# Performance work log

Measured on AMD Instinct MI355X. Metric: run time of the kernel, lower is better.

The kernel has to match this reference:

```python
import jax, jax.numpy as jnp
import numpy as np
import math

B, L, D, H, DFF = 2, 2048, 1024, 16, 4096

def _mha(xq, xkv, Wq, bq, Wk, bk, Wv, bv, Wo, bo, mask, h):
    # xq: [B,Lq,D], xkv: [B,Lk,D], mask: [B,1,Lq,Lk] bool
    b, lq, d = xq.shape
    dk = d // h
    q = (xq @ Wq + bq).reshape(b, lq, h, dk).transpose(0, 2, 1, 3)        # [B,h,Lq,dk]
    k = (xkv @ Wk + bk).reshape(b, -1, h, dk).transpose(0, 2, 1, 3)       # [B,h,Lk,dk]
    v = (xkv @ Wv + bv).reshape(b, -1, h, dk).transpose(0, 2, 1, 3)       # [B,h,Lk,dk]
    scores = jnp.einsum('bhqd,bhkd->bhqk', q, k) / jnp.sqrt(jnp.float32(dk))
    scores = jnp.where(mask, scores, jnp.float32(-1e9))                   # masked_fill(mask==0, -1e9)
    prob = jax.nn.softmax(scores, axis=-1)
    out = jnp.einsum('bhqk,bhkd->bhqd', prob, v)
    out = out.transpose(0, 2, 1, 3).reshape(b, lq, d)
    return out @ Wo + bo

def setup_inputs() -> dict:
    key = jax.random.key(0)
    ks = jax.random.split(key, 16)
    s = 0.02
    inp = {
        'tgt': jax.random.normal(ks[0], (B, L, D), jnp.float32),
        'encoder_out': jax.random.normal(ks[1], (B, L, D), jnp.float32),
        'tgt_mask': jnp.broadcast_to(jnp.tril(jnp.ones((L, L), bool)), (B, 1, L, L)),
        'src_tgt_mask': jnp.ones((B, 1, L, L), bool),
    }
    names = ['sWq','sWk','sWv','sWo','cWq','cWk','cWv','cWo']
    for i, n in enumerate(names):
        inp[n] = s * jax.random.normal(ks[2 + i], (D, D), jnp.float32)
        inp['sb' + n[2] if n[0] == 's' else 'cb' + n[2]] = jnp.zeros((D,), jnp.float32)
    inp['W1'] = s * jax.random.normal(ks[10], (D, DFF), jnp.float32)
    inp['b1'] = jnp.zeros((DFF,), jnp.float32)
    inp['W2'] = s * jax.random.normal(ks[11], (DFF, D), jnp.float32)
    inp['b2'] = jnp.zeros((D,), jnp.float32)
    return inp

def reference(tgt, encoder_out, tgt_mask, src_tgt_mask,
              sWq, sbq, sWk, sbk, sWv, sbv, sWo, sbo,
              cWq, cbq, cWk, cbk, cWv, cbv, cWo, cbo,
              W1, b1, W2, b2):
    # residual 1: masked self-attention (no norm)
    x = tgt + _mha(tgt, tgt, sWq, sbq, sWk, sbk, sWv, sbv, sWo, sbo, tgt_mask, H)
    # residual 2: cross-attention over encoder_out
    x = x + _mha(x, encoder_out, cWq, cbq, cWk, cbk, cWv, cbv, cWo, cbo, src_tgt_mask, H)
    # residual 3: position-wise FFN with ReLU
    x = x + (jax.nn.relu(x @ W1 + b1) @ W2 + b2)
    return x
```

## Files before the change

### kernel.cpp

```cpp
#include <hip/hip_runtime.h>

typedef unsigned short u16;
typedef __attribute__((ext_vector_type(8))) short short8;
typedef __attribute__((ext_vector_type(8))) __bf16 bf16x8;
typedef __attribute__((ext_vector_type(4))) float f32x4;
typedef __attribute__((ext_vector_type(4))) u16 u16x4;

#define GLD16(gp, lp) __builtin_amdgcn_global_load_lds( \
    (const __attribute__((address_space(1))) unsigned int*)(gp), \
    (__attribute__((address_space(3))) unsigned int*)(lp), 16, 0, 0)

__device__ __forceinline__ float bf2f(u16 u){
  unsigned x = ((unsigned)u) << 16; float f; __builtin_memcpy(&f, &x, 4); return f;
}
__device__ __forceinline__ u16 f2bf(float f){
  unsigned x; __builtin_memcpy(&x, &f, 4);
  x += 0x7fffu + ((x >> 16) & 1u);
  return (u16)(x >> 16);
}
__device__ __forceinline__ f32x4 mfma_bf16(short8 a, short8 b, f32x4 c){
  return __builtin_amdgcn_mfma_f32_16x16x32_bf16(
      __builtin_bit_cast(bf16x8, a), __builtin_bit_cast(bf16x8, b), c, 0, 0, 0);
}

__global__ __launch_bounds__(256) void k_conv(const float* __restrict__ s, u16* __restrict__ d, int n){
  int i4 = (blockIdx.x * 256 + threadIdx.x) * 4;
  if (i4 < n){
    float4 v = *(const float4*)(s + i4);
    u16x4 o; o.x = f2bf(v.x); o.y = f2bf(v.y); o.z = f2bf(v.z); o.w = f2bf(v.w);
    *(u16x4*)(d + i4) = o;
  }
}

__global__ __launch_bounds__(256) void k_transpose(const float* __restrict__ s, u16* __restrict__ d, int K, int N){
  __shared__ float t[32][33];
  int bx = blockIdx.x * 32, by = blockIdx.y * 32;
  int x = threadIdx.x & 31, y = threadIdx.x >> 5;
  #pragma unroll
  for (int i = 0; i < 4; i++)
    t[y + i*8][x] = s[(size_t)(by + y + i*8) * N + bx + x];
  __syncthreads();
  #pragma unroll
  for (int i = 0; i < 4; i++)
    d[(size_t)(bx + y + i*8) * K + by + x] = f2bf(t[x][y + i*8]);
}

struct TP8 { const float* s[8]; u16* d[8]; };
__global__ __launch_bounds__(256) void k_transpose8(TP8 p){
  __shared__ float t[32][33];
  const float* s = p.s[blockIdx.z];
  u16* d = p.d[blockIdx.z];
  int bx = blockIdx.x * 32, by = blockIdx.y * 32;
  int x = threadIdx.x & 31, y = threadIdx.x >> 5;
  #pragma unroll
  for (int i = 0; i < 4; i++)
    t[y + i*8][x] = s[(size_t)(by + y + i*8) * 1024 + bx + x];
  __syncthreads();
  #pragma unroll
  for (int i = 0; i < 4; i++)
    d[(size_t)(bx + y + i*8) * 1024 + by + x] = f2bf(t[x][y + i*8]);
}

__global__ __launch_bounds__(256) void k_packbias(
    const float* __restrict__ sbq, const float* __restrict__ sbk,
    const float* __restrict__ sbv, const float* __restrict__ cbk,
    const float* __restrict__ cbv, float* __restrict__ pbS,
    float* __restrict__ pbC){
  int i = blockIdx.x * 256 + threadIdx.x;
  if (i < 3072) pbS[i] = (i < 1024) ? sbq[i] : (i < 2048 ? sbk[i-1024] : sbv[i-2048]);
  if (i < 2048) pbC[i] = (i < 1024) ? cbk[i] : cbv[i-1024];
}

template<int EPI>
__global__ __launch_bounds__(256, 2) void k_gemm_bt(
    const u16* __restrict__ A, const u16* __restrict__ BT,
    const float* __restrict__ bias,
    u16* __restrict__ outB, int M, int N, int K,
    int vt_start, u16* __restrict__ Vt){
  __shared__ u16 As[128*32];
  __shared__ u16 Bs[128*32];
  int tid = threadIdx.x, wave = tid >> 6, lane = tid & 63;
  int bm = blockIdx.x * 128, bn = blockIdx.y * 128;
  int wm = (wave & 1) * 64, wn = (wave >> 1) * 64;
  int l15 = lane & 15, quad = lane >> 4;

  f32x4 z = {0.f, 0.f, 0.f, 0.f};
  f32x4 acc[4][4];
  #pragma unroll
  for (int a = 0; a < 4; a++)
    #pragma unroll
    for (int b = 0; b < 4; b++) acc[a][b] = z;

  int sr = wave*16 + (lane >> 2);
  int sc = (lane & 3) * 8;
  const u16* Ag = A  + (size_t)(bm + sr) * K + sc;
  const u16* Bg = BT + (size_t)(bn + sr) * K + sc;

  for (int k0 = 0; k0 < K; k0 += 32){
    #pragma unroll
    for (int i = 0; i < 2; i++){
      GLD16(Ag + (size_t)i*64*K + k0, &As[(wave*16 + i*64) * 32]);
      GLD16(Bg + (size_t)i*64*K + k0, &Bs[(wave*16 + i*64) * 32]);
    }
    __syncthreads();
    short8 af[4], bf[4];
    #pragma unroll
    for (int mi = 0; mi < 4; mi++)
      af[mi] = *(const short8*)&As[(wm + mi*16 + l15)*32 + quad*8];
    #pragma unroll
    for (int ni = 0; ni < 4; ni++)
      bf[ni] = *(const short8*)&Bs[(wn + ni*16 + l15)*32 + quad*8];
    #pragma unroll
    for (int mi = 0; mi < 4; mi++)
      #pragma unroll
      for (int ni = 0; ni < 4; ni++)
        acc[mi][ni] = mfma_bf16(af[mi], bf[ni], acc[mi][ni]);
    __syncthreads();
  }

  #pragma unroll
  for (int mi = 0; mi < 4; mi++){
    #pragma unroll
    for (int ni = 0; ni < 4; ni++){
      int col = bn + wn + ni*16 + l15;
      float bv = bias[col];
      if (col >= vt_start){
        int vc = col - vt_start;
        int hh = vc >> 6, dd = vc & 63;
        int row0 = bm + wm + mi*16 + quad*4;
        int bb = row0 >> 11, ll = row0 & 2047;
        u16x4 vv;
        #pragma unroll
        for (int r = 0; r < 4; r++) vv[r] = f2bf(acc[mi][ni][r] + bv);
        *(u16x4*)&Vt[(((size_t)bb*16 + hh)*64 + dd)*2048 + ll] = vv;
      } else {
        #pragma unroll
        for (int r = 0; r < 4; r++){
          int row = bm + wm + mi*16 + quad*4 + r;
          float v = acc[mi][ni][r] + bv;
          if (EPI == 1) v = v > 0.f ? v : 0.f;
          outB[(size_t)row * N + col] = f2bf(v);
        }
      }
    }
  }
}

template<int EPI>
__global__ __launch_bounds__(256, 4) void k_gemm_bt64(
    const u16* __restrict__ A, const u16* __restrict__ BT,
    const float* __restrict__ bias, const float* __restrict__ resid,
    float* __restrict__ outF, u16* __restrict__ outB,
    int M, int N, int K){
  __shared__ u16 As[128*32];
  __shared__ u16 Bs[64*32];
  int tid = threadIdx.x, wave = tid >> 6, lane = tid & 63;
  int bm = blockIdx.x * 128, bn = blockIdx.y * 64;
  int wm = wave * 32;
  int l15 = lane & 15, quad = lane >> 4;

  f32x4 z = {0.f, 0.f, 0.f, 0.f};
  f32x4 acc[2][4];
  #pragma unroll
  for (int a = 0; a < 2; a++)
    #pragma unroll
    for (int b = 0; b < 4; b++) acc[a][b] = z;

  int sr = wave*16 + (lane >> 2);
  int sc = (lane & 3) * 8;
  const u16* Ag = A  + (size_t)(bm + sr) * K + sc;
  const u16* Bg = BT + (size_t)(bn + sr) * K + sc;

  for (int k0 = 0; k0 < K; k0 += 32){
    #pragma unroll
    for (int i = 0; i < 2; i++)
      GLD16(Ag + (size_t)i*64*K + k0, &As[(wave*16 + i*64) * 32]);
    GLD16(Bg + k0, &Bs[(wave*16) * 32]);
    __syncthreads();
    short8 af[2], bf[4];
    #pragma unroll
    for (int mi = 0; mi < 2; mi++)
      af[mi] = *(const short8*)&As[(wm + mi*16 + l15)*32 + quad*8];
    #pragma unroll
    for (int ni = 0; ni < 4; ni++)
      bf[ni] = *(const short8*)&Bs[(ni*16 + l15)*32 + quad*8];
    #pragma unroll
    for (int mi = 0; mi < 2; mi++)
      #pragma unroll
      for (int ni = 0; ni < 4; ni++)
        acc[mi][ni] = mfma_bf16(af[mi], bf[ni], acc[mi][ni]);
    __syncthreads();
  }

  #pragma unroll
  for (int mi = 0; mi < 2; mi++){
    #pragma unroll
    for (int ni = 0; ni < 4; ni++){
      int col = bn + ni*16 + l15;
      float bv = bias[col];
      #pragma unroll
      for (int r = 0; r < 4; r++){
        int row = bm + wm + mi*16 + quad*4 + r;
        float v = acc[mi][ni][r] + bv;
        size_t idx = (size_t)row * N + col;
        if (EPI >= 2) v += resid[idx];
        if (EPI == 2 || EPI == 3) outF[idx] = v;
        if (EPI != 3) outB[idx] = f2bf(v);
      }
    }
  }
}

template<bool CAUSAL>
__global__ __launch_bounds__(256, 2) void k_flash(
    const u16* __restrict__ Q, int ldq,
    const u16* __restrict__ Kg, int ldk,
    const u16* __restrict__ Vt,
    u16* __restrict__ O, int ldo){
  __shared__ u16 Ks[128*64];
  __shared__ u16 Vs[64*128];
  __shared__ u16 Ps[128*128];
  int tid = threadIdx.x, wave = tid >> 6, lane = tid & 63;
  int l15 = lane & 15, quad = lane >> 4;
  int qt = blockIdx.x;
  int bh = blockIdx.y;
  int b = bh >> 4, h = bh & 15;
  size_t bL = (size_t)b * 2048;
  const u16* qp = Q  + (bL + qt*128) * (size_t)ldq + h*64;
  const u16* kp = Kg + bL * (size_t)ldk + h*64;
  const u16* vtp = Vt + (size_t)bh * 64 * 2048;
  int wm = wave * 32;

  short8 qf[2][2];
  #pragma unroll
  for (int mi = 0; mi < 2; mi++)
    #pragma unroll
    for (int ks = 0; ks < 2; ks++){
      short8 t = *(const short8*)(qp + (size_t)(wm + mi*16 + l15)*ldq + ks*32 + quad*8);
      #pragma unroll
      for (int j = 0; j < 8; j++)
        t[j] = (short)f2bf(bf2f((u16)t[j]) * 0.125f);
      qf[mi][ks] = t;
    }

  f32x4 z = {0.f, 0.f, 0.f, 0.f};
  f32x4 o[2][4];
  float mrow[2], lrow[2];
  #pragma unroll
  for (int mi = 0; mi < 2; mi++){ mrow[mi] = -3.0e38f; lrow[mi] = 0.f; }
  #pragma unroll
  for (int mi = 0; mi < 2; mi++)
    #pragma unroll
    for (int nd = 0; nd < 4; nd++) o[mi][nd] = z;

  int nkt = CAUSAL ? (qt + 1) : 16;
  for (int kt = 0; kt < nkt; kt++){
    int cg = ((lane & 7) ^ ((lane >> 3) & 7)) * 8;
    #pragma unroll
    for (int i = 0; i < 4; i++){
      int r = i*32 + wave*8 + (lane >> 3);
      GLD16(kp + (size_t)(kt*128 + r) * ldk + cg, &Ks[(i*32 + wave*8) * 64]);
    }
    {
      int d = tid >> 2;
      int cbase = tid & 3;
      const u16* vrow = vtp + (size_t)d*2048 + kt*128;
      short8 vv[4];
      #pragma unroll
      for (int i = 0; i < 4; i++)
        vv[i] = *(const short8*)(vrow + (cbase + i*4)*8);
      #pragma unroll
      for (int i = 0; i < 4; i++){
        int c = cbase + i*4;
        int phys = (c & 8) | ((c ^ (d & 7)) & 7);
        *(short8*)&Vs[d*128 + phys*8] = vv[i];
      }
    }
    __syncthreads();

    f32x4 s[2][8];
    #pragma unroll
    for (int mi = 0; mi < 2; mi++)
      #pragma unroll
      for (int nk = 0; nk < 8; nk++) s[mi][nk] = z;
    #pragma unroll
    for (int ks = 0; ks < 2; ks++){
      short8 kf[8];
      #pragma unroll
      for (int nk = 0; nk < 8; nk++){
        int row = nk*16 + l15;
        kf[nk] = *(const short8*)&Ks[row*64 + (((ks*4 + quad) ^ (row & 7)))*8];
      }
      #pragma unroll
      for (int mi = 0; mi < 2; mi++)
        #pragma unroll
        for (int nk = 0; nk < 8; nk++)
          s[mi][nk] = mfma_bf16(kf[nk], qf[mi][ks], s[mi][nk]);
    }

    if (CAUSAL && kt == qt){
      #pragma unroll
      for (int mi = 0; mi < 2; mi++){
        int q = wm + mi*16 + l15;
        #pragma unroll
        for (int nk = 0; nk < 8; nk++)
          #pragma unroll
          for (int r = 0; r < 4; r++){
            int key = nk*16 + quad*4 + r;
            if (key > q) s[mi][nk][r] = -1e30f;
          }
      }
    }

    #pragma unroll
    for (int mi = 0; mi < 2; mi++){
      float mx = s[mi][0][0];
      #pragma unroll
      for (int nk = 0; nk < 8; nk++)
        #pragma unroll
        for (int r = 0; r < 4; r++) mx = fmaxf(mx, s[mi][nk][r]);
      mx = fmaxf(mx, __shfl_xor(mx, 16));
      mx = fmaxf(mx, __shfl_xor(mx, 32));
      float mnew = fmaxf(mrow[mi], mx);
      float alpha = __expf(mrow[mi] - mnew);
      mrow[mi] = mnew;
      float ls = 0.f;
      #pragma unroll
      for (int nk = 0; nk < 8; nk++)
        #pragma unroll
        for (int r = 0; r < 4; r++){
          float p = __expf(s[mi][nk][r] - mnew);
          s[mi][nk][r] = p;
          ls += p;
        }
      ls += __shfl_xor(ls, 16);
      ls += __shfl_xor(ls, 32);
      lrow[mi] = lrow[mi] * alpha + ls;
      #pragma unroll
      for (int r = 0; r < 4; r++){
        float ar = __shfl(alpha, quad*20 + r);
        #pragma unroll
        for (int nd = 0; nd < 4; nd++) o[mi][nd][r] *= ar;
      }
    }

    #pragma unroll
    for (int mi = 0; mi < 2; mi++){
      int row = wm + mi*16 + l15;
      #pragma unroll
      for (int nk = 0; nk < 8; nk++){
        u16x4 pw;
        #pragma unroll
        for (int r = 0; r < 4; r++) pw[r] = f2bf(s[mi][nk][r]);
        int c = nk*4 + quad;
        int phys = c ^ (row & 14);
        *(u16x4*)&Ps[row*128 + phys*4] = pw;
      }
    }

    #pragma unroll
    for (int kc = 0; kc < 4; kc++){
      short8 vf[4], pf[2];
      #pragma unroll
      for (int nd = 0; nd < 4; nd++){
        int d = nd*16 + l15;
        int cc = kc*4 + quad;
        int phys = (cc & 8) | ((cc ^ (d & 7)) & 7);
        vf[nd] = *(const short8*)&Vs[d*128 + phys*8];
      }
      #pragma unroll
      for (int mi = 0; mi < 2; mi++){
        int row = wm + mi*16 + l15;
        int c = kc*8 + quad*2;
        int phys = c ^ (row & 14);
        pf[mi] = *(const short8*)&Ps[row*128 + phys*4];
      }
      #pragma unroll
      for (int mi = 0; mi < 2; mi++)
        #pragma unroll
        for (int nd = 0; nd < 4; nd++)
          o[mi][nd] = mfma_bf16(pf[mi], vf[nd], o[mi][nd]);
    }
    __syncthreads();
  }

  u16* op = O + (bL + qt*128) * (size_t)ldo + h*64;
  #pragma unroll
  for (int mi = 0; mi < 2; mi++){
    float invl = 1.f / lrow[mi];
    #pragma unroll
    for (int r = 0; r < 4; r++){
      float ir = __shfl(invl, quad*20 + r);
      #pragma unroll
      for (int nd = 0; nd < 4; nd++)
        op[(size_t)(wm + mi*16 + quad*4 + r)*ldo + nd*16 + l15] = f2bf(o[mi][nd][r] * ir);
    }
  }
}

extern "C" void kernel_launch(void* const* d_in, const int* in_sizes, int n_in,
                              void* d_out, int out_size, void* d_ws, size_t ws_size,
                              hipStream_t stream){
  (void)in_sizes; (void)n_in; (void)out_size; (void)ws_size;
  const float* tgt = (const float*)d_in[0];
  const float* enc = (const float*)d_in[1];
  const float* sWq = (const float*)d_in[4];  const float* sbq = (const float*)d_in[5];
  const float* sWk = (const float*)d_in[6];  const float* sbk = (const float*)d_in[7];
  const float* sWv = (const float*)d_in[8];  const float* sbv = (const float*)d_in[9];
  const float* sWo = (const float*)d_in[10]; const float* sbo = (const float*)d_in[11];
  const float* cWq = (const float*)d_in[12]; const float* cbq = (const float*)d_in[13];
  const float* cWk = (const float*)d_in[14]; const float* cbk = (const float*)d_in[15];
  const float* cWv = (const float*)d_in[16]; const float* cbv = (const float*)d_in[17];
  const float* cWo = (const float*)d_in[18]; const float* cbo = (const float*)d_in[19];
  const float* W1  = (const float*)d_in[20]; const float* b1  = (const float*)d_in[21];
  const float* W2  = (const float*)d_in[22]; const float* b2  = (const float*)d_in[23];
  float* out = (float*)d_out;

  const int M = 4096;
  const int NEVER = 1 << 30;
  char* w = (char*)d_ws;
  auto alloc = [&](size_t bytes)->void*{ void* p = w; w += (bytes + 255) & ~(size_t)255; return p; };
  u16* tb    = (u16*)alloc((size_t)M*1024*2);
  u16* eb    = (u16*)alloc((size_t)M*1024*2);
  u16* qkv   = (u16*)alloc((size_t)M*3072*2);
  u16* ao    = (u16*)alloc((size_t)M*1024*2);
  u16* xb    = (u16*)alloc((size_t)M*1024*2);
  float* x1f = (float*)alloc((size_t)M*1024*4);
  u16* hbuf  = (u16*)alloc((size_t)M*4096*2);
  u16* VtS   = (u16*)alloc((size_t)32*64*2048*2);
  u16* VtC   = (u16*)alloc((size_t)32*64*2048*2);
  u16* sQKVT = (u16*)alloc((size_t)3072*1024*2);
  u16* sWoT  = (u16*)alloc((size_t)1024*1024*2);
  u16* cWqT  = (u16*)alloc((size_t)1024*1024*2);
  u16* cKVT  = (u16*)alloc((size_t)2048*1024*2);
  u16* cWoT  = (u16*)alloc((size_t)1024*1024*2);
  u16* W1T   = (u16*)alloc((size_t)4096*1024*2);
  u16* W2T   = (u16*)alloc((size_t)1024*4096*2);
  float* pbS = (float*)alloc(3072*4);
  float* pbC = (float*)alloc(2048*4);
  u16* cq  = tb;
  u16* ckv = qkv;

  k_conv<<<dim3(4096), 256, 0, stream>>>(tgt, tb, M*1024);
  k_conv<<<dim3(4096), 256, 0, stream>>>(enc, eb, M*1024);
  TP8 tp;
  tp.s[0]=sWq; tp.s[1]=sWk; tp.s[2]=sWv; tp.s[3]=sWo;
  tp.s[4]=cWq; tp.s[5]=cWk; tp.s[6]=cWv; tp.s[7]=cWo;
  tp.d[0]=sQKVT; tp.d[1]=sQKVT+1024*1024; tp.d[2]=sQKVT+2048*1024; tp.d[3]=sWoT;
  tp.d[4]=cWqT; tp.d[5]=cKVT; tp.d[6]=cKVT+1024*1024; tp.d[7]=cWoT;
  k_transpose8<<<dim3(32,32,8), 256, 0, stream>>>(tp);
  k_transpose<<<dim3(128,32), 256, 0, stream>>>(W1, W1T, 1024, 4096);
  k_transpose<<<dim3(32,128), 256, 0, stream>>>(W2, W2T, 4096, 1024);
  k_packbias<<<dim3(12), 256, 0, stream>>>(sbq, sbk, sbv, cbk, cbv, pbS, pbC);

  k_gemm_bt<0><<<dim3(32,24), 256, 0, stream>>>(tb, sQKVT, pbS, qkv, M, 3072, 1024, 2048, VtS);
  k_flash<true><<<dim3(16,32), 256, 0, stream>>>(qkv, 3072, qkv+1024, 3072, VtS, ao, 1024);
  k_gemm_bt64<2><<<dim3(32,16), 256, 0, stream>>>(ao, sWoT, sbo, tgt, x1f, xb, M, 1024, 1024);

  k_gemm_bt64<0><<<dim3(32,16), 256, 0, stream>>>(xb, cWqT, cbq, nullptr, nullptr, cq, M, 1024, 1024);
  k_gemm_bt<0><<<dim3(32,16), 256, 0, stream>>>(eb, cKVT, pbC, ckv, M, 2048, 1024, 1024, VtC);
  k_flash<false><<<dim3(16,32), 256, 0, stream>>>(cq, 1024, ckv, 2048, VtC, ao, 1024);
  k_gemm_bt64<2><<<dim3(32,16), 256, 0, stream>>>(ao, cWoT, cbo, x1f, x1f, xb, M, 1024, 1024);

  k_gemm_bt<1><<<dim3(32,32), 256, 0, stream>>>(xb, W1T, b1, hbuf, M, 4096, 1024, NEVER, nullptr);
  k_gemm_bt64<3><<<dim3(32,16), 256, 0, stream>>>(hbuf, W2T, b2, x1f, out, nullptr, M, 1024, 4096);
}
```

Baseline: 589.8 us.

## Double-buffer GEMM, unify N=1024 GEMMs, and tune flash softmax and loads

Makes the 128x128 GEMM double-buffered in LDS, issuing the next K-tile's global-to-LDS loads before computing on the current one so only one barrier per iteration remains. The 128x64 GEMM is removed and the N=1024 projections run on the 128x128 kernel with residual epilogues. In flash attention, log2(e) is folded into the Q scale so softmax uses raw exp2, P is packed to bf16 by truncation via perm instead of round-to-nearest, V tiles are loaded with direct global-to-LDS loads, and causal query tiles are interleaved to balance work. Larger tiles for the N=1024 GEMMs mean fewer blocks (256 versus 512) and more LDS per block, and truncating P slightly changes numerics.

```diff
diff --git a/kernel.cpp b/kernel.cpp
--- a/kernel.cpp
+++ b/kernel.cpp
@@ -1,14 +1,25 @@
 #include <hip/hip_runtime.h>
 
 typedef unsigned short u16;
+typedef unsigned int u32;
 typedef __attribute__((ext_vector_type(8))) short short8;
 typedef __attribute__((ext_vector_type(8))) __bf16 bf16x8;
 typedef __attribute__((ext_vector_type(4))) float f32x4;
 typedef __attribute__((ext_vector_type(4))) u16 u16x4;
+typedef __attribute__((ext_vector_type(2))) u32 u32x2;
 
 #define GLD16(gp, lp) __builtin_amdgcn_global_load_lds( \
     (const __attribute__((address_space(1))) unsigned int*)(gp), \
     (__attribute__((address_space(3))) unsigned int*)(lp), 16, 0, 0)
+
+#if defined(__has_builtin) && __has_builtin(__builtin_amdgcn_exp2f)
+#define EXP2(x) __builtin_amdgcn_exp2f(x)
+#else
+static __device__ __forceinline__ float exp2_asm(float x){
+  float r; asm("v_exp_f32 %0, %1" : "=v"(r) : "v"(x)); return r;
+}
+#define EXP2(x) exp2_asm(x)
+#endif
 
 __device__ __forceinline__ float bf2f(u16 u){
   unsigned x = ((unsigned)u) << 16; float f; __builtin_memcpy(&f, &x, 4); return f;
@@ -17,6 +28,10 @@
   unsigned x; __builtin_memcpy(&x, &f, 4);
   x += 0x7fffu + ((x >> 16) & 1u);
   return (u16)(x >> 16);
+}
+__device__ __forceinline__ u32 pkhi(float lo, float hi){
+  u32 a, b; __builtin_memcpy(&a, &lo, 4); __builtin_memcpy(&b, &hi, 4);
+  return __builtin_amdgcn_perm(b, a, 0x07060302u);
 }
 __device__ __forceinline__ f32x4 mfma_bf16(short8 a, short8 b, f32x4 c){
   return __builtin_amdgcn_mfma_f32_16x16x32_bf16(
@@ -74,11 +89,11 @@
 template<int EPI>
 __global__ __launch_bounds__(256, 2) void k_gemm_bt(
     const u16* __restrict__ A, const u16* __restrict__ BT,
-    const float* __restrict__ bias,
-    u16* __restrict__ outB, int M, int N, int K,
-    int vt_start, u16* __restrict__ Vt){
-  __shared__ u16 As[128*32];
-  __shared__ u16 Bs[128*32];
+    const float* __restrict__ bias, const float* __restrict__ resid,
+    float* __restrict__ outF, u16* __restrict__ outB,
+    int M, int N, int K, int vt_start, u16* __restrict__ Vt){
+  __shared__ u16 As[2][128*32];
+  __shared__ u16 Bs[2][128*32];
   int tid = threadIdx.x, wave = tid >> 6, lane = tid & 63;
   int bm = blockIdx.x * 128, bn = blockIdx.y * 128;
   int wm = (wave & 1) * 64, wn = (wave >> 1) * 64;
@@ -95,27 +110,35 @@
   int sc = (lane & 3) * 8;
   const u16* Ag = A  + (size_t)(bm + sr) * K + sc;
   const u16* Bg = BT + (size_t)(bn + sr) * K + sc;
-
-  for (int k0 = 0; k0 < K; k0 += 32){
-    #pragma unroll
-    for (int i = 0; i < 2; i++){
-      GLD16(Ag + (size_t)i*64*K + k0, &As[(wave*16 + i*64) * 32]);
-      GLD16(Bg + (size_t)i*64*K + k0, &Bs[(wave*16 + i*64) * 32]);
-    }
+  int NK = K >> 5;
+
+  GLD16(Ag,                 &As[0][(wave*16     ) * 32]);
+  GLD16(Ag + (size_t)64*K,  &As[0][(wave*16 + 64) * 32]);
+  GLD16(Bg,                 &Bs[0][(wave*16     ) * 32]);
+  GLD16(Bg + (size_t)64*K,  &Bs[0][(wave*16 + 64) * 32]);
+
+  for (int kt = 0; kt < NK; kt++){
     __syncthreads();
+    int cur = kt & 1;
+    if (kt + 1 < NK){
+      int nb = cur ^ 1, k0 = (kt + 1) * 32;
+      GLD16(Ag + k0,                &As[nb][(wave*16     ) * 32]);
+      GLD16(Ag + (size_t)64*K + k0, &As[nb][(wave*16 + 64) * 32]);
+      GLD16(Bg + k0,                &Bs[nb][(wave*16     ) * 32]);
+      GLD16(Bg + (size_t)64*K + k0, &Bs[nb][(wave*16 + 64) * 32]);
+    }
     short8 af[4], bf[4];
     #pragma unroll
     for (int mi = 0; mi < 4; mi++)
-      af[mi] = *(const short8*)&As[(wm + mi*16 + l15)*32 + quad*8];
+      af[mi] = *(const short8*)&As[cur][(wm + mi*16 + l15)*32 + quad*8];
     #pragma unroll
     for (int ni = 0; ni < 4; ni++)
-      bf[ni] = *(const short8*)&Bs[(wn + ni*16 + l15)*32 + quad*8];
+      bf[ni] = *(const short8*)&Bs[cur][(wn + ni*16 + l15)*32 + quad*8];
     #pragma unroll
     for (int mi = 0; mi < 4; mi++)
       #pragma unroll
       for (int ni = 0; ni < 4; ni++)
         acc[mi][ni] = mfma_bf16(af[mi], bf[ni], acc[mi][ni]);
-    __syncthreads();
   }
 
   #pragma unroll
@@ -124,7 +147,7 @@
     for (int ni = 0; ni < 4; ni++){
       int col = bn + wn + ni*16 + l15;
       float bv = bias[col];
-      if (col >= vt_start){
+      if (EPI == 0 && col >= vt_start){
         int vc = col - vt_start;
         int hh = vc >> 6, dd = vc & 63;
         int row0 = bm + wm + mi*16 + quad*4;
@@ -139,73 +162,11 @@
           int row = bm + wm + mi*16 + quad*4 + r;
           float v = acc[mi][ni][r] + bv;
           if (EPI == 1) v = v > 0.f ? v : 0.f;
-          outB[(size_t)row * N + col] = f2bf(v);
+          size_t idx = (size_t)row * N + col;
+          if (EPI >= 2) v += resid[idx];
+          if (EPI == 2 || EPI == 3) outF[idx] = v;
+          if (EPI != 3) outB[idx] = f2bf(v);
         }
-      }
-    }
-  }
-}
-
-template<int EPI>
-__global__ __launch_bounds__(256, 4) void k_gemm_bt64(
-    const u16* __restrict__ A, const u16* __restrict__ BT,
-    const float* __restrict__ bias, const float* __restrict__ resid,
-    float* __restrict__ outF, u16* __restrict__ outB,
-    int M, int N, int K){
-  __shared__ u16 As[128*32];
-  __shared__ u16 Bs[64*32];
-  int tid = threadIdx.x, wave = tid >> 6, lane = tid & 63;
-  int bm = blockIdx.x * 128, bn = blockIdx.y * 64;
-  int wm = wave * 32;
-  int l15 = lane & 15, quad = lane >> 4;
-
-  f32x4 z = {0.f, 0.f, 0.f, 0.f};
-  f32x4 acc[2][4];
-  #pragma unroll
-  for (int a = 0; a < 2; a++)
-    #pragma unroll
-    for (int b = 0; b < 4; b++) acc[a][b] = z;
-
-  int sr = wave*16 + (lane >> 2);
-  int sc = (lane & 3) * 8;
-  const u16* Ag = A  + (size_t)(bm + sr) * K + sc;
-  const u16* Bg = BT + (size_t)(bn + sr) * K + sc;
-
-  for (int k0 = 0; k0 < K; k0 += 32){
-    #pragma unroll
-    for (int i = 0; i < 2; i++)
-      GLD16(Ag + (size_t)i*64*K + k0, &As[(wave*16 + i*64) * 32]);
-    GLD16(Bg + k0, &Bs[(wave*16) * 32]);
-    __syncthreads();
-    short8 af[2], bf[4];
-    #pragma unroll
-    for (int mi = 0; mi < 2; mi++)
-      af[mi] = *(const short8*)&As[(wm + mi*16 + l15)*32 + quad*8];
-    #pragma unroll
-    for (int ni = 0; ni < 4; ni++)
-      bf[ni] = *(const short8*)&Bs[(ni*16 + l15)*32 + quad*8];
-    #pragma unroll
-    for (int mi = 0; mi < 2; mi++)
-      #pragma unroll
-      for (int ni = 0; ni < 4; ni++)
-        acc[mi][ni] = mfma_bf16(af[mi], bf[ni], acc[mi][ni]);
-    __syncthreads();
-  }
-
-  #pragma unroll
-  for (int mi = 0; mi < 2; mi++){
-    #pragma unroll
-    for (int ni = 0; ni < 4; ni++){
-      int col = bn + ni*16 + l15;
-      float bv = bias[col];
-      #pragma unroll
-      for (int r = 0; r < 4; r++){
-        int row = bm + wm + mi*16 + quad*4 + r;
-        float v = acc[mi][ni][r] + bv;
-        size_t idx = (size_t)row * N + col;
-        if (EPI >= 2) v += resid[idx];
-        if (EPI == 2 || EPI == 3) outF[idx] = v;
-        if (EPI != 3) outB[idx] = f2bf(v);
       }
     }
   }
@@ -222,7 +183,8 @@
   __shared__ u16 Ps[128*128];
   int tid = threadIdx.x, wave = tid >> 6, lane = tid & 63;
   int l15 = lane & 15, quad = lane >> 4;
-  int qt = blockIdx.x;
+  int bx = blockIdx.x;
+  int qt = CAUSAL ? ((bx & 1) ? (15 - (bx >> 1)) : (bx >> 1)) : bx;
   int bh = blockIdx.y;
   int b = bh >> 4, h = bh & 15;
   size_t bL = (size_t)b * 2048;
@@ -231,6 +193,7 @@
   const u16* vtp = Vt + (size_t)bh * 64 * 2048;
   int wm = wave * 32;
 
+  const float QSCALE = 0.125f * 1.44269504088896f;
   short8 qf[2][2];
   #pragma unroll
   for (int mi = 0; mi < 2; mi++)
@@ -239,7 +202,7 @@
       short8 t = *(const short8*)(qp + (size_t)(wm + mi*16 + l15)*ldq + ks*32 + quad*8);
       #pragma unroll
       for (int j = 0; j < 8; j++)
-        t[j] = (short)f2bf(bf2f((u16)t[j]) * 0.125f);
+        t[j] = (short)f2bf(bf2f((u16)t[j]) * QSCALE);
       qf[mi][ks] = t;
     }
 
@@ -261,20 +224,13 @@
       int r = i*32 + wave*8 + (lane >> 3);
       GLD16(kp + (size_t)(kt*128 + r) * ldk + cg, &Ks[(i*32 + wave*8) * 64]);
     }
-    {
-      int d = tid >> 2;
-      int cbase = tid & 3;
-      const u16* vrow = vtp + (size_t)d*2048 + kt*128;
-      short8 vv[4];
-      #pragma unroll
-      for (int i = 0; i < 4; i++)
-        vv[i] = *(const short8*)(vrow + (cbase + i*4)*8);
-      #pragma unroll
-      for (int i = 0; i < 4; i++){
-        int c = cbase + i*4;
-        int phys = (c & 8) | ((c ^ (d & 7)) & 7);
-        *(short8*)&Vs[d*128 + phys*8] = vv[i];
-      }
+    #pragma unroll
+    for (int i = 0; i < 4; i++){
+      int d0 = i*16 + wave*4;
+      int d = d0 + (lane >> 4);
+      int j = lane & 15;
+      int chunk = (j & 8) | ((j ^ (d & 7)) & 7);
+      GLD16(vtp + (size_t)d*2048 + kt*128 + chunk*8, &Vs[d0*128]);
     }
     __syncthreads();
 
@@ -322,14 +278,14 @@
       mx = fmaxf(mx, __shfl_xor(mx, 16));
       mx = fmaxf(mx, __shfl_xor(mx, 32));
       float mnew = fmaxf(mrow[mi], mx);
-      float alpha = __expf(mrow[mi] - mnew);
+      float alpha = EXP2(mrow[mi] - mnew);
       mrow[mi] = mnew;
       float ls = 0.f;
       #pragma unroll
       for (int nk = 0; nk < 8; nk++)
         #pragma unroll
         for (int r = 0; r < 4; r++){
-          float p = __expf(s[mi][nk][r] - mnew);
+          float p = EXP2(s[mi][nk][r] - mnew);
           s[mi][nk][r] = p;
           ls += p;
         }
@@ -349,12 +305,12 @@
       int row = wm + mi*16 + l15;
       #pragma unroll
       for (int nk = 0; nk < 8; nk++){
-        u16x4 pw;
-        #pragma unroll
-        for (int r = 0; r < 4; r++) pw[r] = f2bf(s[mi][nk][r]);
+        u32x2 pw;
+        pw.x = pkhi(s[mi][nk][0], s[mi][nk][1]);
+        pw.y = pkhi(s[mi][nk][2], s[mi][nk][3]);
         int c = nk*4 + quad;
         int phys = c ^ (row & 14);
-        *(u16x4*)&Ps[row*128 + phys*4] = pw;
+        *(u32x2*)&Ps[row*128 + phys*4] = pw;
       }
     }
 
@@ -453,15 +409,15 @@
   k_transpose<<<dim3(32,128), 256, 0, stream>>>(W2, W2T, 4096, 1024);
   k_packbias<<<dim3(12), 256, 0, stream>>>(sbq, sbk, sbv, cbk, cbv, pbS, pbC);
 
-  k_gemm_bt<0><<<dim3(32,24), 256, 0, stream>>>(tb, sQKVT, pbS, qkv, M, 3072, 1024, 2048, VtS);
+  k_gemm_bt<0><<<dim3(32,24), 256, 0, stream>>>(tb, sQKVT, pbS, nullptr, nullptr, qkv, M, 3072, 1024, 2048, VtS);
   k_flash<true><<<dim3(16,32), 256, 0, stream>>>(qkv, 3072, qkv+1024, 3072, VtS, ao, 1024);
-  k_gemm_bt64<2><<<dim3(32,16), 256, 0, stream>>>(ao, sWoT, sbo, tgt, x1f, xb, M, 1024, 1024);
-
-  k_gemm_bt64<0><<<dim3(32,16), 256, 0, stream>>>(xb, cWqT, cbq, nullptr, nullptr, cq, M, 1024, 1024);
-  k_gemm_bt<0><<<dim3(32,16), 256, 0, stream>>>(eb, cKVT, pbC, ckv, M, 2048, 1024, 1024, VtC);
+  k_gemm_bt<2><<<dim3(32,8), 256, 0, stream>>>(ao, sWoT, sbo, tgt, x1f, xb, M, 1024, 1024, NEVER, nullptr);
+
+  k_gemm_bt<0><<<dim3(32,8), 256, 0, stream>>>(xb, cWqT, cbq, nullptr, nullptr, cq, M, 1024, 1024, NEVER, nullptr);
+  k_gemm_bt<0><<<dim3(32,16), 256, 0, stream>>>(eb, cKVT, pbC, nullptr, nullptr, ckv, M, 2048, 1024, 1024, VtC);
   k_flash<false><<<dim3(16,32), 256, 0, stream>>>(cq, 1024, ckv, 2048, VtC, ao, 1024);
-  k_gemm_bt64<2><<<dim3(32,16), 256, 0, stream>>>(ao, cWoT, cbo, x1f, x1f, xb, M, 1024, 1024);
-
-  k_gemm_bt<1><<<dim3(32,32), 256, 0, stream>>>(xb, W1T, b1, hbuf, M, 4096, 1024, NEVER, nullptr);
-  k_gemm_bt64<3><<<dim3(32,16), 256, 0, stream>>>(hbuf, W2T, b2, x1f, out, nullptr, M, 1024, 4096);
-}
+  k_gemm_bt<2><<<dim3(32,8), 256, 0, stream>>>(ao, cWoT, cbo, x1f, x1f, xb, M, 1024, 1024, NEVER, nullptr);
+
+  k_gemm_bt<1><<<dim3(32,32), 256, 0, stream>>>(xb, W1T, b1, nullptr, nullptr, hbuf, M, 4096, 1024, NEVER, nullptr);
+  k_gemm_bt<3><<<dim3(32,8), 256, 0, stream>>>(hbuf, W2T, b2, x1f, out, nullptr, M, 1024, 4096, NEVER, nullptr);
+}
```

After: 575.2 us. -2.5%, faster.
